# Kernel tuning notes

Hardware: AMD Instinct MI355X
Metric: run time of the kernel (lower is better)

Reference implementation:

```python
import jax, jax.numpy as jnp
import numpy as np

B, N, DIN, DOUT = 1, 8192, 256, 256
EPS = 1e-8

def setup_inputs() -> dict:
    key = jax.random.key(0)
    kA, kX, k1, k2, k3, k4 = jax.random.split(key, 6)
    A = jax.random.uniform(kA, (B, N, N), dtype=jnp.float32)          # dense adjacency [B,N,N]
    X = jax.random.normal(kX, (B, N, DIN), dtype=jnp.float32)          # node features [B,N,Din]
    s1 = 1.0 / np.sqrt(DIN)
    s2 = 1.0 / np.sqrt(DIN + DOUT)
    W_w = jax.random.uniform(k1, (DIN, DOUT), jnp.float32, -s1, s1)
    b_w = jax.random.uniform(k2, (DOUT,), jnp.float32, -s1, s1)
    W_fc = jax.random.uniform(k3, (DIN + DOUT, DOUT), jnp.float32, -s2, s2)
    b_fc = jax.random.uniform(k4, (DOUT,), jnp.float32, -s2, s2)
    return {"A": A, "X": X, "W_w": W_w, "b_w": b_w, "W_fc": W_fc, "b_fc": b_fc}

def reference(A, X, W_w, b_w, W_fc, b_fc):
    # inputs = relu(weight(X))  [B,N,Dout]
    h = jax.nn.relu(jnp.einsum('bnd,de->bne', X, W_w) + b_w)
    # A[...,None] * inputs[:,None] summed over neighbor dim == matmul (avg pooling)
    pooled = jnp.einsum('bij,bjd->bid', A, h)                # [B,N,Dout]
    size = jnp.sum(A, axis=2, keepdims=True) + EPS           # [B,N,1]
    pooled = pooled / size
    cat = jnp.concatenate([X, pooled], axis=-1)              # [B,N,Din+Dout]
    out = jax.nn.relu(jnp.einsum('bnd,de->bne', cat, W_fc) + b_fc) + EPS
    out = out / (jnp.linalg.norm(out) + EPS)                 # global L2 norm over all elements
    return out
```

## Files before the change

kernel.cpp:

```cpp
#include <hip/hip_runtime.h>
#include <hip/hip_bf16.h>
#include <math.h>

typedef __bf16 bf16;
typedef bf16 bf16x8 __attribute__((ext_vector_type(8)));
typedef bf16 bf16x4 __attribute__((ext_vector_type(4)));
typedef float f32x4 __attribute__((ext_vector_type(4)));

#define N_NODES 8192
#define DIN 256
#define DOUT 256
#define KCAT 512
#define EPSF 1e-8f
#define KSPLIT 4
#define KBLK 2048
#define BM 128
#define BK 32
#define NT (KBLK / BK)
#define STAGE 24576
#define BBASE 8192

__device__ __forceinline__ f32x4 mfma16(bf16x8 a, bf16x8 b, f32x4 c) {
    return __builtin_amdgcn_mfma_f32_16x16x32_bf16(a, b, c, 0, 0, 0);
}

#define WAITVM(N) asm volatile("s_waitcnt vmcnt(" #N ")" ::: "memory")
#define WAITLGKM  asm volatile("s_waitcnt lgkmcnt(0)" ::: "memory")
#define BAR       __builtin_amdgcn_s_barrier()

__global__ __launch_bounds__(256) void k0_prep(const float* __restrict__ Ww,
                                               const float* __restrict__ Wfc,
                                               bf16* __restrict__ WwT,
                                               bf16* __restrict__ WfcT) {
    int tid = blockIdx.x * 256 + threadIdx.x;
    if (tid < 256 * 256) {
        int n = tid >> 8, k = tid & 255;
        WwT[n * 256 + k] = (bf16)Ww[k * 256 + n];
    }
    if (tid < 256 * 512) {
        int n = tid >> 9, k = tid & 511;
        WfcT[n * 512 + k] = (bf16)Wfc[k * 256 + n];
    }
}

__global__ __launch_bounds__(128) void k1_h(const float* __restrict__ X,
                                            const bf16* __restrict__ WwT,
                                            const float* __restrict__ bw,
                                            bf16* __restrict__ hT) {
    const int lane = threadIdx.x & 63;
    const int wid  = threadIdx.x >> 6;
    const int m0   = blockIdx.x * 16;
    const int lrow = lane & 15;
    const int lk8  = (lane >> 4) * 8;

    f32x4 acc[8];
#pragma unroll
    for (int i = 0; i < 8; ++i) acc[i] = {0.f, 0.f, 0.f, 0.f};

#pragma unroll
    for (int ks = 0; ks < DIN; ks += 32) {
        const float* xp = X + (size_t)(m0 + lrow) * DIN + ks + lk8;
        f32x4 x0 = *reinterpret_cast<const f32x4*>(xp);
        f32x4 x1 = *reinterpret_cast<const f32x4*>(xp + 4);
        bf16x8 a;
#pragma unroll
        for (int j = 0; j < 4; ++j) { a[j] = (bf16)x0[j]; a[4 + j] = (bf16)x1[j]; }
#pragma unroll
        for (int nb = 0; nb < 8; ++nb) {
            int col = wid * 128 + nb * 16 + lrow;
            bf16x8 b = *reinterpret_cast<const bf16x8*>(WwT + (size_t)col * DIN + ks + lk8);
            acc[nb] = mfma16(a, b, acc[nb]);
        }
    }
    const int mrow = m0 + (lane >> 4) * 4;
#pragma unroll
    for (int nb = 0; nb < 8; ++nb) {
        int col = wid * 128 + nb * 16 + lrow;
        float bias = bw[col];
        bf16x4 hv;
#pragma unroll
        for (int j = 0; j < 4; ++j) {
            float v = acc[nb][j] + bias;
            hv[j] = (bf16)(v > 0.f ? v : 0.f);
        }
        *reinterpret_cast<bf16x4*>(hT + (size_t)col * N_NODES + mrow) = hv;
    }
}

__global__ __launch_bounds__(512, 2) void k2_pool(const float* __restrict__ A,
                                                  const bf16* __restrict__ hT,
                                                  float* __restrict__ part,
                                                  float* __restrict__ rsG) {
    __shared__ __align__(16) unsigned char lds[4][STAGE];
    __shared__ float rsp[4][BM];
    const int t    = threadIdx.x;
    const int lane = t & 63;
    const int wid  = t >> 6;
    const int wr   = wid >> 2;
    const int wn   = wid & 3;
    const int lrow = lane & 15;
    const int lk4  = lane >> 4;
    const int mblk = blockIdx.x & 63;
    const int ks   = blockIdx.x >> 6;
    const int m0   = mblk * BM;
    const int kbase = ks * KBLK;

    f32x4 acc[4][4];
    f32x4 sums[4];
#pragma unroll
    for (int i = 0; i < 4; ++i) {
        sums[i] = {0.f, 0.f, 0.f, 0.f};
#pragma unroll
        for (int j = 0; j < 4; ++j) acc[i][j] = {0.f, 0.f, 0.f, 0.f};
    }
    bf16x8 bOne;
#pragma unroll
    for (int j = 0; j < 8; ++j) bOne[j] = (bf16)1.0f;

    const int arow = t >> 2;
    const int aseg = t & 3;
    const float* aSrc = A + (size_t)(m0 + arow) * N_NODES + kbase + aseg * 8;
    const int awb = arow * 64 + ((aseg ^ ((arow >> 1) & 3)) << 4);

    const bf16* bsrc[2];
    int bdst[2];
#pragma unroll
    for (int r = 0; r < 2; ++r) {
        int idx = r * 512 + t;
        int col = idx >> 2;
        int gs  = (idx & 3) ^ ((col >> 1) & 3);
        bsrc[r] = hT + (size_t)col * N_NODES + kbase + gs * 8;
        bdst[r] = BBASE + r * 8192 + wid * 1024;
    }

    int aOff[4], bOff[4];
#pragma unroll
    for (int mf = 0; mf < 4; ++mf) {
        int row = wr * 64 + mf * 16 + lrow;
        aOff[mf] = row * 64 + ((lk4 ^ ((row >> 1) & 3)) << 4);
    }
#pragma unroll
    for (int nf = 0; nf < 4; ++nf) {
        int col = wn * 64 + nf * 16 + lrow;
        bOff[nf] = BBASE + col * 64 + ((lk4 ^ ((col >> 1) & 3)) << 4);
    }

    f32x4 rlo[3], rhi[3];

#define ALOAD(set, tile) do {                                                 \
        const float* p_ = aSrc + (size_t)(tile) * BK;                         \
        rlo[set] = *reinterpret_cast<const f32x4*>(p_);                       \
        rhi[set] = *reinterpret_cast<const f32x4*>(p_ + 4);                   \
    } while (0)

#define CVTWRITE(set, bufidx) do {                                            \
        bf16x8 w_;                                                            \
        _Pragma("unroll")                                                     \
        for (int j = 0; j < 4; ++j) {                                         \
            w_[j] = (bf16)rlo[set][j]; w_[4 + j] = (bf16)rhi[set][j];         \
        }                                                                     \
        *reinterpret_cast<bf16x8*>(&lds[bufidx][awb]) = w_;                   \
    } while (0)

#define BDMA(tile, bufidx) do {                                               \
        _Pragma("unroll")                                                     \
        for (int r_ = 0; r_ < 2; ++r_) {                                      \
            __builtin_amdgcn_global_load_lds(                                 \
                (const __attribute__((address_space(1))) void*)(bsrc[r_] + (size_t)(tile) * BK), \
                (__attribute__((address_space(3))) void*)&lds[bufidx][bdst[r_]], \
                16, 0, 0);                                                    \
        }                                                                     \
    } while (0)

#define COMPUTE(bufidx, tile) do {                                            \
        bf16x8 af_[4], bf_[4];                                                \
        _Pragma("unroll")                                                     \
        for (int f = 0; f < 4; ++f)                                           \
            af_[f] = *reinterpret_cast<const bf16x8*>(&lds[bufidx][aOff[f]]); \
        _Pragma("unroll")                                                     \
        for (int f = 0; f < 4; ++f)                                           \
            bf_[f] = *reinterpret_cast<const bf16x8*>(&lds[bufidx][bOff[f]]); \
        _Pragma("unroll")                                                     \
        for (int mf = 0; mf < 4; ++mf)                                        \
            _Pragma("unroll")                                                 \
            for (int nf = 0; nf < 4; ++nf)                                    \
                acc[mf][nf] = mfma16(af_[mf], bf_[nf], acc[mf][nf]);          \
        if (wn == ((tile) & 3)) {                                             \
            _Pragma("unroll")                                                 \
            for (int mf = 0; mf < 4; ++mf)                                    \
                sums[mf] = mfma16(af_[mf], bOne, sums[mf]);                   \
        }                                                                     \
    } while (0)

    ALOAD(0, 0); BDMA(0, 0);
    ALOAD(1, 1); BDMA(1, 1);
    ALOAD(2, 2); BDMA(2, 2);
    CVTWRITE(0, 0);
    ALOAD(0, 3);
    WAITVM(10);
    WAITLGKM;
    BAR;

    for (int tt = 0; tt < NT - 3; ++tt) {
        CVTWRITE((tt + 1) % 3, (tt + 1) & 3);
        COMPUTE(tt & 3, tt);
        BDMA(tt + 3, (tt + 3) & 3);
        ALOAD((tt + 1) % 3, (tt + 4 < NT) ? (tt + 4) : 0);
        WAITVM(10);
        WAITLGKM;
        BAR;
    }
    CVTWRITE((NT - 2) % 3, (NT - 2) & 3);
    COMPUTE((NT - 3) & 3, NT - 3);
    WAITVM(6);
    WAITLGKM;
    BAR;
    CVTWRITE((NT - 1) % 3, (NT - 1) & 3);
    COMPUTE((NT - 2) & 3, NT - 2);
    WAITVM(2);
    WAITLGKM;
    BAR;
    COMPUTE((NT - 1) & 3, NT - 1);

    __syncthreads();
    if (lrow == 0) {
#pragma unroll
        for (int mf = 0; mf < 4; ++mf)
#pragma unroll
            for (int j = 0; j < 4; ++j)
                rsp[wn][wr * 64 + mf * 16 + lk4 * 4 + j] = sums[mf][j];
    }
    __syncthreads();
    if (t < BM)
        rsG[(size_t)ks * N_NODES + m0 + t] = rsp[0][t] + rsp[1][t] + rsp[2][t] + rsp[3][t];

    float* pp = part + ((size_t)ks * N_NODES + m0) * DOUT;
#pragma unroll
    for (int mf = 0; mf < 4; ++mf)
#pragma unroll
        for (int nf = 0; nf < 4; ++nf) {
            int col = wn * 64 + nf * 16 + lrow;
#pragma unroll
            for (int j = 0; j < 4; ++j) {
                int row = wr * 64 + mf * 16 + lk4 * 4 + j;
                pp[(size_t)row * DOUT + col] = acc[mf][nf][j];
            }
        }
#undef ALOAD
#undef CVTWRITE
#undef BDMA
#undef COMPUTE
}

__global__ __launch_bounds__(128) void k3_out(const float* __restrict__ X,
                                              const float* __restrict__ part,
                                              const float* __restrict__ rsG,
                                              const bf16* __restrict__ WfcT,
                                              const float* __restrict__ bfc,
                                              float* __restrict__ out,
                                              float* __restrict__ partials) {
    const int lane = threadIdx.x & 63;
    const int wid  = threadIdx.x >> 6;
    const int m0   = blockIdx.x * 16;
    const int lrow = lane & 15;
    const int lk8  = (lane >> 4) * 8;

    f32x4 acc[8];
#pragma unroll
    for (int i = 0; i < 8; ++i) acc[i] = {0.f, 0.f, 0.f, 0.f};

    float rs = EPSF;
#pragma unroll
    for (int sp = 0; sp < KSPLIT; ++sp) rs += rsG[(size_t)sp * N_NODES + m0 + lrow];
    const float inv = 1.f / rs;

#pragma unroll
    for (int ksx = 0; ksx < 256; ksx += 32) {
        const float* xp = X + (size_t)(m0 + lrow) * DIN + ksx + lk8;
        f32x4 x0 = *reinterpret_cast<const f32x4*>(xp);
        f32x4 x1 = *reinterpret_cast<const f32x4*>(xp + 4);
        bf16x8 a;
#pragma unroll
        for (int j = 0; j < 4; ++j) { a[j] = (bf16)x0[j]; a[4 + j] = (bf16)x1[j]; }
#pragma unroll
        for (int nb = 0; nb < 8; ++nb) {
            int col = wid * 128 + nb * 16 + lrow;
            bf16x8 b = *reinterpret_cast<const bf16x8*>(WfcT + (size_t)col * KCAT + ksx + lk8);
            acc[nb] = mfma16(a, b, acc[nb]);
        }
    }
#pragma unroll
    for (int ksx = 256; ksx < 512; ksx += 32) {
        f32x4 s0 = {0.f, 0.f, 0.f, 0.f}, s1 = {0.f, 0.f, 0.f, 0.f};
#pragma unroll
        for (int sp = 0; sp < KSPLIT; ++sp) {
            const float* pp = part + ((size_t)sp * N_NODES + m0 + lrow) * DOUT + (ksx - 256) + lk8;
            f32x4 v0 = *reinterpret_cast<const f32x4*>(pp);
            f32x4 v1 = *reinterpret_cast<const f32x4*>(pp + 4);
#pragma unroll
            for (int j = 0; j < 4; ++j) { s0[j] += v0[j]; s1[j] += v1[j]; }
        }
        bf16x8 a;
#pragma unroll
        for (int j = 0; j < 4; ++j) { a[j] = (bf16)(s0[j] * inv); a[4 + j] = (bf16)(s1[j] * inv); }
#pragma unroll
        for (int nb = 0; nb < 8; ++nb) {
            int col = wid * 128 + nb * 16 + lrow;
            bf16x8 b = *reinterpret_cast<const bf16x8*>(WfcT + (size_t)col * KCAT + ksx + lk8);
            acc[nb] = mfma16(a, b, acc[nb]);
        }
    }

    float ss = 0.f;
#pragma unroll
    for (int nb = 0; nb < 8; ++nb) {
        int col = wid * 128 + nb * 16 + lrow;
        float bias = bfc[col];
#pragma unroll
        for (int j = 0; j < 4; ++j) {
            int row = m0 + (lane >> 4) * 4 + j;
            float v = acc[nb][j] + bias;
            v = (v > 0.f ? v : 0.f) + EPSF;
            out[(size_t)row * DOUT + col] = v;
            ss += v * v;
        }
    }
#pragma unroll
    for (int off = 32; off; off >>= 1) ss += __shfl_xor(ss, off);
    __shared__ float sw[2];
    if (lane == 0) sw[wid] = ss;
    __syncthreads();
    if (threadIdx.x == 0) partials[blockIdx.x] = sw[0] + sw[1];
}

__global__ __launch_bounds__(256) void k4_norm(float* __restrict__ out,
                                               const float* __restrict__ partials) {
    __shared__ float sw[4];
    float s = partials[threadIdx.x] + partials[threadIdx.x + 256];
#pragma unroll
    for (int off = 32; off; off >>= 1) s += __shfl_xor(s, off);
    if ((threadIdx.x & 63) == 0) sw[threadIdx.x >> 6] = s;
    __syncthreads();
    float total = sw[0] + sw[1] + sw[2] + sw[3];
    float scale = 1.f / (sqrtf(total) + EPSF);
    f32x4* o4 = reinterpret_cast<f32x4*>(out);
    const int nvec = N_NODES * DOUT / 4;
    for (int i = blockIdx.x * blockDim.x + threadIdx.x; i < nvec; i += gridDim.x * blockDim.x) {
        f32x4 v = o4[i];
#pragma unroll
        for (int j = 0; j < 4; ++j) v[j] *= scale;
        o4[i] = v;
    }
}

extern "C" void kernel_launch(void* const* d_in, const int* in_sizes, int n_in,
                              void* d_out, int out_size, void* d_ws, size_t ws_size,
                              hipStream_t stream) {
    const float* A   = (const float*)d_in[0];
    const float* X   = (const float*)d_in[1];
    const float* Ww  = (const float*)d_in[2];
    const float* bw  = (const float*)d_in[3];
    const float* Wfc = (const float*)d_in[4];
    const float* bfc = (const float*)d_in[5];
    float* out = (float*)d_out;

    char* ws = (char*)d_ws;
    bf16*  hT        = (bf16*)(ws);
    bf16*  WwT       = (bf16*)(ws + (8u << 20));
    bf16*  WfcT      = (bf16*)(ws + (8u << 20) + (128u << 10));
    float* partials  = (float*)(ws + (8u << 20) + (384u << 10));
    float* rsG       = (float*)(ws + (8u << 20) + (512u << 10));
    float* part      = (float*)(ws + (16u << 20));

    k0_prep<<<512, 256, 0, stream>>>(Ww, Wfc, WwT, WfcT);
    k1_h<<<512, 128, 0, stream>>>(X, WwT, bw, hT);
    k2_pool<<<256, 512, 0, stream>>>(A, hT, part, rsG);
    k3_out<<<512, 128, 0, stream>>>(X, part, rsG, WfcT, bfc, out, partials);
    k4_norm<<<256, 256, 0, stream>>>(out, partials);
}
```

Before: 168.9 us.

## Double K-split in pooling kernel, shrink pipeline to double buffer, fp32 row sums

```diff
diff --git a/kernel.cpp b/kernel.cpp
--- a/kernel.cpp
+++ b/kernel.cpp
@@ -12,12 +12,12 @@
 #define DOUT 256
 #define KCAT 512
 #define EPSF 1e-8f
-#define KSPLIT 4
-#define KBLK 2048
+#define KSPLIT 8
+#define KBLK 1024
 #define BM 128
 #define BK 32
 #define NT (KBLK / BK)
-#define STAGE 24576
+#define BUFSZ 24576
 #define BBASE 8192
 
 __device__ __forceinline__ f32x4 mfma16(bf16x8 a, bf16x8 b, f32x4 c) {
@@ -87,12 +87,11 @@
     }
 }
 
-__global__ __launch_bounds__(512, 2) void k2_pool(const float* __restrict__ A,
+__global__ __launch_bounds__(512, 4) void k2_pool(const float* __restrict__ A,
                                                   const bf16* __restrict__ hT,
                                                   float* __restrict__ part,
                                                   float* __restrict__ rsG) {
-    __shared__ __align__(16) unsigned char lds[4][STAGE];
-    __shared__ float rsp[4][BM];
+    __shared__ __align__(16) unsigned char lds[2][BUFSZ];
     const int t    = threadIdx.x;
     const int lane = t & 63;
     const int wid  = t >> 6;
@@ -106,16 +105,12 @@
     const int kbase = ks * KBLK;
 
     f32x4 acc[4][4];
-    f32x4 sums[4];
-#pragma unroll
-    for (int i = 0; i < 4; ++i) {
-        sums[i] = {0.f, 0.f, 0.f, 0.f};
+#pragma unroll
+    for (int i = 0; i < 4; ++i)
 #pragma unroll
         for (int j = 0; j < 4; ++j) acc[i][j] = {0.f, 0.f, 0.f, 0.f};
-    }
-    bf16x8 bOne;
-#pragma unroll
-    for (int j = 0; j < 8; ++j) bOne[j] = (bf16)1.0f;
+
+    float rsum = 0.f;
 
     const int arow = t >> 2;
     const int aseg = t & 3;
@@ -145,19 +140,21 @@
         bOff[nf] = BBASE + col * 64 + ((lk4 ^ ((col >> 1) & 3)) << 4);
     }
 
-    f32x4 rlo[3], rhi[3];
-
-#define ALOAD(set, tile) do {                                                 \
+    f32x4 ra0, ra1;
+
+#define ALOAD(tile) do {                                                      \
         const float* p_ = aSrc + (size_t)(tile) * BK;                         \
-        rlo[set] = *reinterpret_cast<const f32x4*>(p_);                       \
-        rhi[set] = *reinterpret_cast<const f32x4*>(p_ + 4);                   \
+        ra0 = *reinterpret_cast<const f32x4*>(p_);                            \
+        ra1 = *reinterpret_cast<const f32x4*>(p_ + 4);                        \
     } while (0)
 
-#define CVTWRITE(set, bufidx) do {                                            \
+#define CVTW(bufidx) do {                                                     \
         bf16x8 w_;                                                            \
         _Pragma("unroll")                                                     \
-        for (int j = 0; j < 4; ++j) {                                         \
-            w_[j] = (bf16)rlo[set][j]; w_[4 + j] = (bf16)rhi[set][j];         \
+        for (int j_ = 0; j_ < 4; ++j_) {                                      \
+            w_[j_]     = (bf16)ra0[j_];                                       \
+            w_[4 + j_] = (bf16)ra1[j_];                                       \
+            rsum += ra0[j_] + ra1[j_];                                        \
         }                                                                     \
         *reinterpret_cast<bf16x8*>(&lds[bufidx][awb]) = w_;                   \
     } while (0)
@@ -172,67 +169,46 @@
         }                                                                     \
     } while (0)
 
-#define COMPUTE(bufidx, tile) do {                                            \
+#define COMPUTE(bufidx) do {                                                  \
         bf16x8 af_[4], bf_[4];                                                \
         _Pragma("unroll")                                                     \
-        for (int f = 0; f < 4; ++f)                                           \
+        for (int f = 0; f < 4; ++f) {                                         \
             af_[f] = *reinterpret_cast<const bf16x8*>(&lds[bufidx][aOff[f]]); \
-        _Pragma("unroll")                                                     \
-        for (int f = 0; f < 4; ++f)                                           \
             bf_[f] = *reinterpret_cast<const bf16x8*>(&lds[bufidx][bOff[f]]); \
+        }                                                                     \
         _Pragma("unroll")                                                     \
         for (int mf = 0; mf < 4; ++mf)                                        \
             _Pragma("unroll")                                                 \
             for (int nf = 0; nf < 4; ++nf)                                    \
                 acc[mf][nf] = mfma16(af_[mf], bf_[nf], acc[mf][nf]);          \
-        if (wn == ((tile) & 3)) {                                             \
-            _Pragma("unroll")                                                 \
-            for (int mf = 0; mf < 4; ++mf)                                    \
-                sums[mf] = mfma16(af_[mf], bOne, sums[mf]);                   \
-        }                                                                     \
     } while (0)
 
-    ALOAD(0, 0); BDMA(0, 0);
-    ALOAD(1, 1); BDMA(1, 1);
-    ALOAD(2, 2); BDMA(2, 2);
-    CVTWRITE(0, 0);
-    ALOAD(0, 3);
-    WAITVM(10);
+    ALOAD(0); BDMA(0, 0);
+    CVTW(0);
+    ALOAD(1); BDMA(1, 1);
+    WAITVM(4);
     WAITLGKM;
     BAR;
 
-    for (int tt = 0; tt < NT - 3; ++tt) {
-        CVTWRITE((tt + 1) % 3, (tt + 1) & 3);
-        COMPUTE(tt & 3, tt);
-        BDMA(tt + 3, (tt + 3) & 3);
-        ALOAD((tt + 1) % 3, (tt + 4 < NT) ? (tt + 4) : 0);
-        WAITVM(10);
+    for (int tt = 0; tt < NT - 2; ++tt) {
+        CVTW((tt + 1) & 1);
+        COMPUTE(tt & 1);
+        ALOAD(tt + 2);
+        WAITVM(2);
         WAITLGKM;
         BAR;
-    }
-    CVTWRITE((NT - 2) % 3, (NT - 2) & 3);
-    COMPUTE((NT - 3) & 3, NT - 3);
-    WAITVM(6);
+        BDMA(tt + 2, tt & 1);
+    }
+    CVTW((NT - 1) & 1);
+    COMPUTE((NT - 2) & 1);
+    WAITVM(0);
     WAITLGKM;
     BAR;
-    CVTWRITE((NT - 1) % 3, (NT - 1) & 3);
-    COMPUTE((NT - 2) & 3, NT - 2);
-    WAITVM(2);
-    WAITLGKM;
-    BAR;
-    COMPUTE((NT - 1) & 3, NT - 1);
-
-    __syncthreads();
-    if (lrow == 0) {
-#pragma unroll
-        for (int mf = 0; mf < 4; ++mf)
-#pragma unroll
-            for (int j = 0; j < 4; ++j)
-                rsp[wn][wr * 64 + mf * 16 + lk4 * 4 + j] = sums[mf][j];
-    }
-    __syncthreads();
-    if (t < BM)
-        rsG[(size_t)ks * N_NODES + m0 + t] = rsp[0][t] + rsp[1][t] + rsp[2][t] + rsp[3][t];
+    COMPUTE((NT - 1) & 1);
+
+    rsum += __shfl_xor(rsum, 1);
+    rsum += __shfl_xor(rsum, 2);
+    if ((t & 3) == 0) rsG[(size_t)ks * N_NODES + m0 + arow] = rsum;
 
     float* pp = part + ((size_t)ks * N_NODES + m0) * DOUT;
 #pragma unroll
@@ -247,7 +223,7 @@
             }
         }
 #undef ALOAD
-#undef CVTWRITE
+#undef CVTW
 #undef BDMA
 #undef COMPUTE
 }
@@ -374,7 +350,7 @@
 
     k0_prep<<<512, 256, 0, stream>>>(Ww, Wfc, WwT, WfcT);
     k1_h<<<512, 128, 0, stream>>>(X, WwT, bw, hT);
-    k2_pool<<<256, 512, 0, stream>>>(A, hT, part, rsG);
+    k2_pool<<<512, 512, 0, stream>>>(A, hT, part, rsG);
     k3_out<<<512, 128, 0, stream>>>(X, part, rsG, WfcT, bfc, out, partials);
     k4_norm<<<256, 256, 0, stream>>>(out, partials);
 }
```

After: 171.2 us. About the same (+1.3%).
